# Performance work log

Hardware: AMD Instinct MI355X
Metric: run time of the kernel (lower is better)

Reference implementation:

```python
import jax, jax.numpy as jnp
import numpy as np

B, L, HID = 4, 1024, 768
H, D = 12, 64  # num heads, head dim (HID = H*D)


def setup_inputs() -> dict:
    key = jax.random.key(0)
    ks = jax.random.split(key, 8)
    s = 0.02
    return {
        "hidden_states": jax.random.normal(ks[0], (B, L, HID), jnp.float32),
        "attention_mask": jnp.zeros((B, 1, 1, L), jnp.float32),
        "structure_matrix": jax.random.normal(ks[1], (L, L, D), jnp.float32) * s,
        "Wq": jax.random.normal(ks[2], (HID, HID), jnp.float32) * s,
        "bq": jnp.zeros((HID,), jnp.float32),
        "Wk": jax.random.normal(ks[3], (HID, HID), jnp.float32) * s,
        "bk": jnp.zeros((HID,), jnp.float32),
        "Wv": jax.random.normal(ks[4], (HID, HID), jnp.float32) * s,
        "bv": jnp.zeros((HID,), jnp.float32),
    }


def _heads(x):
    # [B, L, HID] -> [B, H, L, D]
    return x.reshape(B, L, H, D).transpose(0, 2, 1, 3)


def reference(hidden_states, attention_mask, structure_matrix, Wq, bq, Wk, bk, Wv, bv):
    q = _heads(hidden_states @ Wq.T + bq)  # bhld
    k = _heads(hidden_states @ Wk.T + bk)
    v = _heads(hidden_states @ Wv.T + bv)
    scores = jnp.einsum('bhld,bhrd->bhlr', q, k)
    # structure bias: query-side and key-side position-pair terms
    scores = scores + jnp.einsum('bhld,lrd->bhlr', q, structure_matrix)
    scores = scores + jnp.einsum('bhrd,lrd->bhlr', k, structure_matrix)
    scores = scores / jnp.sqrt(jnp.asarray(D, scores.dtype))
    scores = scores + attention_mask
    probs = jax.nn.softmax(scores, axis=-1)
    ctx = jnp.einsum('bhlr,bhrd->bhld', probs, v)
    return ctx.transpose(0, 2, 1, 3).reshape(B, L, HID)
```

## Files before the change

### kernel.cpp

```cpp
#include <hip/hip_runtime.h>

#define BATCH 4
#define SEQ   1024
#define HIDN  768
#define NH    12
#define HD    64
#define BHN   48

typedef __attribute__((ext_vector_type(8))) short bf16x8;
typedef __attribute__((ext_vector_type(4))) float f32x4;

#define MFMA(a, b, c) __builtin_amdgcn_mfma_f32_16x16x32_bf16((a), (b), (c), 0, 0, 0)

__device__ inline unsigned short f2bf(float f) {
    union { float f; unsigned u; } v; v.f = f;
    unsigned r = (v.u + 0x7FFFu + ((v.u >> 16) & 1u)) >> 16;
    return (unsigned short)r;
}
__device__ inline float bf2f(unsigned short s) {
    union { unsigned u; float f; } v; v.u = ((unsigned)s) << 16;
    return v.f;
}
__device__ inline unsigned long long pack4(float a, float b, float c, float d) {
    return (unsigned long long)f2bf(a)
         | ((unsigned long long)f2bf(b) << 16)
         | ((unsigned long long)f2bf(c) << 32)
         | ((unsigned long long)f2bf(d) << 48);
}

__global__ __launch_bounds__(256) void qkv_kernel(
    const float* __restrict__ hidden,
    const float* __restrict__ Wq, const float* __restrict__ bq,
    const float* __restrict__ Wk, const float* __restrict__ bk,
    const float* __restrict__ Wv, const float* __restrict__ bv,
    unsigned short* __restrict__ Qb, unsigned short* __restrict__ Kb,
    unsigned short* __restrict__ Vb)
{
    const int mt  = blockIdx.x;
    const int nt  = blockIdx.y;
    const int mat = blockIdx.z;
    const float* W  = (mat == 0) ? Wq : (mat == 1) ? Wk : Wv;
    const float* bs = (mat == 0) ? bq : (mat == 1) ? bk : bv;
    unsigned short* out = (mat == 0) ? Qb : (mat == 1) ? Kb : Vb;

    const int t = threadIdx.x, lane = t & 63, wid = t >> 6;
    const int row16 = lane & 15, kg = lane >> 4;
    const int m0 = mt * 128;
    const int wm = (wid >> 1) * 64, wn = (wid & 1) * 32;

    __shared__ __align__(16) unsigned short As[128 * 40];
    __shared__ __align__(16) unsigned short Ws[64 * 40];

    f32x4 acc[4][2] = {};

    for (int k0 = 0; k0 < HIDN; k0 += 32) {
        for (int i = 0; i < 4; ++i) {
            int f4 = t + i * 256;
            int r = f4 >> 3, c4 = f4 & 7;
            float4 v = *(const float4*)(hidden + (size_t)(m0 + r) * HIDN + k0 + c4 * 4);
            *(unsigned long long*)&As[r * 40 + c4 * 4] = pack4(v.x, v.y, v.z, v.w);
        }
        for (int i = 0; i < 2; ++i) {
            int f4 = t + i * 256;
            int r = f4 >> 3, c4 = f4 & 7;
            float4 v = *(const float4*)(W + (size_t)(nt * 64 + r) * HIDN + k0 + c4 * 4);
            *(unsigned long long*)&Ws[r * 40 + c4 * 4] = pack4(v.x, v.y, v.z, v.w);
        }
        __syncthreads();
        bf16x8 af[4], bfr[2];
        for (int mf = 0; mf < 4; ++mf)
            af[mf] = *(const bf16x8*)&As[(wm + mf * 16 + row16) * 40 + kg * 8];
        for (int nf = 0; nf < 2; ++nf)
            bfr[nf] = *(const bf16x8*)&Ws[(wn + nf * 16 + row16) * 40 + kg * 8];
        for (int mf = 0; mf < 4; ++mf)
            for (int nf = 0; nf < 2; ++nf)
                acc[mf][nf] = MFMA(af[mf], bfr[nf], acc[mf][nf]);
        __syncthreads();
    }

    const int bh = (m0 / SEQ) * NH + nt;
    for (int nf = 0; nf < 2; ++nf) {
        int d = wn + nf * 16 + row16;
        float bias_v = bs[nt * 64 + d];
        for (int mf = 0; mf < 4; ++mf)
            for (int j = 0; j < 4; ++j) {
                int m = m0 + wm + mf * 16 + kg * 4 + j;
                int l = m & (SEQ - 1);
                out[((size_t)bh * SEQ + l) * HD + d] = f2bf(acc[mf][nf][j] + bias_v);
            }
    }
}

__global__ __launch_bounds__(512) void scores_kernel(
    const float* __restrict__ sm, const float* __restrict__ mask,
    const unsigned short* __restrict__ Qb, const unsigned short* __restrict__ Kb,
    float* __restrict__ S)
{
    const int rt = blockIdx.x, lt = blockIdx.y;
    const int r0 = rt * 32, l0 = lt * 16;
    const int t = threadIdx.x, lane = t & 63, wid = t >> 6;
    const int row16 = lane & 15, kg = lane >> 4;

    __shared__ __align__(16) unsigned short sm_s[16 * 32 * 64];
    __shared__ __align__(16) unsigned short bias_s[16 * 32 * 48];
    __shared__ float mask_s[BATCH * 32];

    for (int i = 0; i < 16; ++i) {
        int f4 = t + i * 512;
        int l = f4 >> 9;
        int rem = f4 & 511;
        int r = rem >> 4, d4 = rem & 15;
        float4 v = *(const float4*)(sm + ((size_t)(l0 + l) * SEQ + (r0 + r)) * HD + d4 * 4);
        int idx = (((l * 32 + r) * 64) + d4 * 4) ^ ((((l ^ r) & 7) << 3));
        *(unsigned long long*)&sm_s[idx] = pack4(v.x, v.y, v.z, v.w);
    }
    if (t < BATCH * 32) {
        int b = t >> 5, r = t & 31;
        mask_s[t] = mask[(size_t)b * SEQ + r0 + r];
    }
    __syncthreads();

    for (int li = 0; li < 2; ++li) {
        int l = wid * 2 + li;
        bf16x8 af[2][2];
        for (int mf = 0; mf < 2; ++mf)
            for (int kf = 0; kf < 2; ++kf) {
                int r = mf * 16 + row16, d0 = kf * 32 + kg * 8;
                af[mf][kf] = *(const bf16x8*)&sm_s[(((l * 32 + r) * 64) + d0) ^ ((((l ^ r) & 7) << 3))];
            }
        bf16x8 bq8[3][2];
        for (int nf = 0; nf < 3; ++nf)
            for (int kf = 0; kf < 2; ++kf) {
                int bh = nf * 16 + row16, d0 = kf * 32 + kg * 8;
                bq8[nf][kf] = *(const bf16x8*)&Qb[((size_t)bh * SEQ + l0 + l) * HD + d0];
            }
        f32x4 acc[2][3] = {};
        for (int kf = 0; kf < 2; ++kf)
            for (int mf = 0; mf < 2; ++mf)
                for (int nf = 0; nf < 3; ++nf)
                    acc[mf][nf] = MFMA(af[mf][kf], bq8[nf][kf], acc[mf][nf]);
        for (int mf = 0; mf < 2; ++mf)
            for (int nf = 0; nf < 3; ++nf)
                for (int j = 0; j < 4; ++j) {
                    int r = mf * 16 + kg * 4 + j, bh = nf * 16 + row16;
                    bias_s[(l * 32 + r) * 48 + bh] = f2bf(acc[mf][nf][j]);
                }
    }
    __syncthreads();

    for (int ri = 0; ri < 4; ++ri) {
        int r = wid * 4 + ri;
        bf16x8 af[2];
        for (int kf = 0; kf < 2; ++kf) {
            int l = row16, d0 = kf * 32 + kg * 8;
            af[kf] = *(const bf16x8*)&sm_s[(((l * 32 + r) * 64) + d0) ^ ((((l ^ r) & 7) << 3))];
        }
        bf16x8 bk8[3][2];
        for (int nf = 0; nf < 3; ++nf)
            for (int kf = 0; kf < 2; ++kf) {
                int bh = nf * 16 + row16, d0 = kf * 32 + kg * 8;
                bk8[nf][kf] = *(const bf16x8*)&Kb[((size_t)bh * SEQ + r0 + r) * HD + d0];
            }
        f32x4 acc[3] = {};
        for (int kf = 0; kf < 2; ++kf)
            for (int nf = 0; nf < 3; ++nf)
                acc[nf] = MFMA(af[kf], bk8[nf][kf], acc[nf]);
        for (int nf = 0; nf < 3; ++nf)
            for (int j = 0; j < 4; ++j) {
                int l = kg * 4 + j, bh = nf * 16 + row16;
                int idx = (l * 32 + r) * 48 + bh;
                bias_s[idx] = f2bf(bf2f(bias_s[idx]) + acc[nf][j]);
            }
    }
    __syncthreads();

    for (int bi = 0; bi < 6; ++bi) {
        int bh = wid * 6 + bi;
        int b = bh / NH;
        bf16x8 aq[2], bkf[2][2];
        for (int kf = 0; kf < 2; ++kf)
            aq[kf] = *(const bf16x8*)&Qb[((size_t)bh * SEQ + l0 + row16) * HD + kf * 32 + kg * 8];
        for (int nf = 0; nf < 2; ++nf)
            for (int kf = 0; kf < 2; ++kf)
                bkf[nf][kf] = *(const bf16x8*)&Kb[((size_t)bh * SEQ + r0 + nf * 16 + row16) * HD + kf * 32 + kg * 8];
        f32x4 acc[2] = {};
        for (int kf = 0; kf < 2; ++kf)
            for (int nf = 0; nf < 2; ++nf)
                acc[nf] = MFMA(aq[kf], bkf[nf][kf], acc[nf]);
        for (int nf = 0; nf < 2; ++nf) {
            int r = nf * 16 + row16;
            for (int j = 0; j < 4; ++j) {
                int l = kg * 4 + j;
                float s = (acc[nf][j] + bf2f(bias_s[(l * 32 + r) * 48 + bh])) * 0.125f
                        + mask_s[b * 32 + r];
                S[((size_t)bh * SEQ + l0 + l) * SEQ + r0 + r] = s;
            }
        }
    }
}

__global__ __launch_bounds__(256) void softmax_kernel(float* __restrict__ S)
{
    const int row = blockIdx.x;
    float* base = S + (size_t)row * SEQ;
    const int t = threadIdx.x;

    float4 v = ((const float4*)base)[t];
    float m = fmaxf(fmaxf(v.x, v.y), fmaxf(v.z, v.w));
    for (int off = 32; off; off >>= 1) m = fmaxf(m, __shfl_xor(m, off));
    __shared__ float red[4], red2[4];
    if ((t & 63) == 0) red[t >> 6] = m;
    __syncthreads();
    m = fmaxf(fmaxf(red[0], red[1]), fmaxf(red[2], red[3]));

    float e0 = __expf(v.x - m), e1 = __expf(v.y - m);
    float e2 = __expf(v.z - m), e3 = __expf(v.w - m);
    float s = e0 + e1 + e2 + e3;
    for (int off = 32; off; off >>= 1) s += __shfl_xor(s, off);
    if ((t & 63) == 0) red2[t >> 6] = s;
    __syncthreads();
    s = red2[0] + red2[1] + red2[2] + red2[3];
    float inv = 1.0f / s;

    ((unsigned long long*)base)[t] = pack4(e0 * inv, e1 * inv, e2 * inv, e3 * inv);
}

__global__ __launch_bounds__(256) void pv_kernel(
    const float* __restrict__ Sbuf, const unsigned short* __restrict__ Vb,
    float* __restrict__ out)
{
    const int bh = blockIdx.x;
    const int l0 = blockIdx.y * 128;
    const int b = bh / NH, h = bh % NH;
    const int t = threadIdx.x, lane = t & 63, wid = t >> 6;
    const int row16 = lane & 15, kg = lane >> 4;
    const int wm = (wid >> 1) * 64, wn = (wid & 1) * 32;

    __shared__ __align__(16) unsigned short pt[128 * 72];
    __shared__ __align__(16) unsigned short vt[64 * 72];
    const unsigned short* P = (const unsigned short*)Sbuf;

    f32x4 acc[4][2] = {};
    for (int r0 = 0; r0 < SEQ; r0 += 64) {
        for (int i = 0; i < 8; ++i) {
            int f4 = t + i * 256;
            int row = f4 >> 4, c4 = f4 & 15;
            *(unsigned long long*)&pt[row * 72 + c4 * 4] =
                *(const unsigned long long*)&P[((size_t)(bh * SEQ + l0 + row)) * 2048 + r0 + c4 * 4];
        }
        for (int i = 0; i < 4; ++i) {
            int f4 = t + i * 256;
            int r = f4 >> 4, c4 = f4 & 15;
            unsigned long long pk =
                *(const unsigned long long*)&Vb[((size_t)bh * SEQ + r0 + r) * HD + c4 * 4];
            vt[(c4 * 4 + 0) * 72 + r] = (unsigned short)(pk);
            vt[(c4 * 4 + 1) * 72 + r] = (unsigned short)(pk >> 16);
            vt[(c4 * 4 + 2) * 72 + r] = (unsigned short)(pk >> 32);
            vt[(c4 * 4 + 3) * 72 + r] = (unsigned short)(pk >> 48);
        }
        __syncthreads();
        for (int kf = 0; kf < 2; ++kf) {
            int kk = kf * 32 + kg * 8;
            bf16x8 af[4], bfr[2];
            for (int mf = 0; mf < 4; ++mf)
                af[mf] = *(const bf16x8*)&pt[(wm + mf * 16 + row16) * 72 + kk];
            for (int nf = 0; nf < 2; ++nf)
                bfr[nf] = *(const bf16x8*)&vt[(wn + nf * 16 + row16) * 72 + kk];
            for (int mf = 0; mf < 4; ++mf)
                for (int nf = 0; nf < 2; ++nf)
                    acc[mf][nf] = MFMA(af[mf], bfr[nf], acc[mf][nf]);
        }
        __syncthreads();
    }

    for (int nf = 0; nf < 2; ++nf) {
        int d = wn + nf * 16 + row16;
        for (int mf = 0; mf < 4; ++mf)
            for (int j = 0; j < 4; ++j) {
                int l = l0 + wm + mf * 16 + kg * 4 + j;
                out[((size_t)(b * SEQ + l)) * HIDN + h * HD + d] = acc[mf][nf][j];
            }
    }
}

extern "C" void kernel_launch(void* const* d_in, const int* in_sizes, int n_in,
                              void* d_out, int out_size, void* d_ws, size_t ws_size,
                              hipStream_t stream)
{
    const float* hidden = (const float*)d_in[0];
    const float* mask   = (const float*)d_in[1];
    const float* smat   = (const float*)d_in[2];
    const float* Wq = (const float*)d_in[3];
    const float* bq = (const float*)d_in[4];
    const float* Wk = (const float*)d_in[5];
    const float* bk = (const float*)d_in[6];
    const float* Wv = (const float*)d_in[7];
    const float* bv = (const float*)d_in[8];
    float* out = (float*)d_out;

    char* ws = (char*)d_ws;
    unsigned short* Qb = (unsigned short*)(ws);
    unsigned short* Kb = (unsigned short*)(ws + 6291456);
    unsigned short* Vb = (unsigned short*)(ws + 12582912);
    float* S = (float*)(ws + 18874368);

    qkv_kernel<<<dim3(32, 12, 3), 256, 0, stream>>>(hidden, Wq, bq, Wk, bk, Wv, bv, Qb, Kb, Vb);
    scores_kernel<<<dim3(32, 64), 512, 0, stream>>>(smat, mask, Qb, Kb, S);
    softmax_kernel<<<dim3(BHN * SEQ), 256, 0, stream>>>(S);
    pv_kernel<<<dim3(BHN, 8), 256, 0, stream>>>(S, Vb, out);
}
```

Before: 688.9 us.

## Fuse softmax into PV kernel and shrink scores tile to 16x16

Softmax is merged into the P·V kernel: each block reads 16 fp32 score rows, normalizes them in registers, and keeps bf16 probabilities in a swizzled LDS tile. This removes the separate softmax pass and its bf16 write and re-read of P. V tiles are double-buffered in LDS. The scores kernel tile drops from 32 to 16 key columns with a transposed, padded bias layout and an occupancy hint, doubling the grid. The cost is that V is re-staged by 64 small blocks per head instead of 8, and each PV block does far less MFMA work.

```diff
diff --git a/kernel.cpp b/kernel.cpp
--- a/kernel.cpp
+++ b/kernel.cpp
@@ -91,69 +91,66 @@
     }
 }
 
-__global__ __launch_bounds__(512) void scores_kernel(
+__global__ __launch_bounds__(512, 4) void scores_kernel(
     const float* __restrict__ sm, const float* __restrict__ mask,
     const unsigned short* __restrict__ Qb, const unsigned short* __restrict__ Kb,
     float* __restrict__ S)
 {
     const int rt = blockIdx.x, lt = blockIdx.y;
-    const int r0 = rt * 32, l0 = lt * 16;
+    const int r0 = rt * 16, l0 = lt * 16;
     const int t = threadIdx.x, lane = t & 63, wid = t >> 6;
     const int row16 = lane & 15, kg = lane >> 4;
 
-    __shared__ __align__(16) unsigned short sm_s[16 * 32 * 64];
-    __shared__ __align__(16) unsigned short bias_s[16 * 32 * 48];
-    __shared__ float mask_s[BATCH * 32];
-
-    for (int i = 0; i < 16; ++i) {
+    __shared__ __align__(16) unsigned short sm_s[16 * 16 * 64];
+    __shared__ __align__(16) unsigned short bias_s[16 * 48 * 18];
+    __shared__ float mask_s[BATCH * 16];
+
+    for (int i = 0; i < 8; ++i) {
         int f4 = t + i * 512;
-        int l = f4 >> 9;
-        int rem = f4 & 511;
+        int l = f4 >> 8;
+        int rem = f4 & 255;
         int r = rem >> 4, d4 = rem & 15;
         float4 v = *(const float4*)(sm + ((size_t)(l0 + l) * SEQ + (r0 + r)) * HD + d4 * 4);
-        int idx = (((l * 32 + r) * 64) + d4 * 4) ^ ((((l ^ r) & 7) << 3));
+        int idx = ((l * 16 + r) * 64 + d4 * 4) ^ (((l ^ r) & 7) << 3);
         *(unsigned long long*)&sm_s[idx] = pack4(v.x, v.y, v.z, v.w);
     }
-    if (t < BATCH * 32) {
-        int b = t >> 5, r = t & 31;
+    if (t < BATCH * 16) {
+        int b = t >> 4, r = t & 15;
         mask_s[t] = mask[(size_t)b * SEQ + r0 + r];
     }
     __syncthreads();
 
     for (int li = 0; li < 2; ++li) {
         int l = wid * 2 + li;
-        bf16x8 af[2][2];
-        for (int mf = 0; mf < 2; ++mf)
-            for (int kf = 0; kf < 2; ++kf) {
-                int r = mf * 16 + row16, d0 = kf * 32 + kg * 8;
-                af[mf][kf] = *(const bf16x8*)&sm_s[(((l * 32 + r) * 64) + d0) ^ ((((l ^ r) & 7) << 3))];
-            }
+        bf16x8 af[2];
+        for (int kf = 0; kf < 2; ++kf) {
+            int d0 = kf * 32 + kg * 8;
+            af[kf] = *(const bf16x8*)&sm_s[((l * 16 + row16) * 64 + d0) ^ (((l ^ row16) & 7) << 3)];
+        }
         bf16x8 bq8[3][2];
         for (int nf = 0; nf < 3; ++nf)
             for (int kf = 0; kf < 2; ++kf) {
                 int bh = nf * 16 + row16, d0 = kf * 32 + kg * 8;
                 bq8[nf][kf] = *(const bf16x8*)&Qb[((size_t)bh * SEQ + l0 + l) * HD + d0];
             }
-        f32x4 acc[2][3] = {};
+        f32x4 acc[3] = {};
         for (int kf = 0; kf < 2; ++kf)
-            for (int mf = 0; mf < 2; ++mf)
-                for (int nf = 0; nf < 3; ++nf)
-                    acc[mf][nf] = MFMA(af[mf][kf], bq8[nf][kf], acc[mf][nf]);
-        for (int mf = 0; mf < 2; ++mf)
             for (int nf = 0; nf < 3; ++nf)
-                for (int j = 0; j < 4; ++j) {
-                    int r = mf * 16 + kg * 4 + j, bh = nf * 16 + row16;
-                    bias_s[(l * 32 + r) * 48 + bh] = f2bf(acc[mf][nf][j]);
-                }
-    }
-    __syncthreads();
-
-    for (int ri = 0; ri < 4; ++ri) {
-        int r = wid * 4 + ri;
+                acc[nf] = MFMA(af[kf], bq8[nf][kf], acc[nf]);
+        for (int nf = 0; nf < 3; ++nf)
+            for (int j = 0; j < 4; ++j) {
+                int r = kg * 4 + j, bh = nf * 16 + row16;
+                bias_s[(l * 48 + bh) * 18 + r] = f2bf(acc[nf][j]);
+            }
+    }
+    __syncthreads();
+
+    for (int ri = 0; ri < 2; ++ri) {
+        int r = wid * 2 + ri;
         bf16x8 af[2];
         for (int kf = 0; kf < 2; ++kf) {
-            int l = row16, d0 = kf * 32 + kg * 8;
-            af[kf] = *(const bf16x8*)&sm_s[(((l * 32 + r) * 64) + d0) ^ ((((l ^ r) & 7) << 3))];
+            int d0 = kf * 32 + kg * 8;
+            af[kf] = *(const bf16x8*)&sm_s[((row16 * 16 + r) * 64 + d0) ^ (((row16 ^ r) & 7) << 3)];
         }
         bf16x8 bk8[3][2];
         for (int nf = 0; nf < 3; ++nf)
@@ -168,7 +165,7 @@
         for (int nf = 0; nf < 3; ++nf)
             for (int j = 0; j < 4; ++j) {
                 int l = kg * 4 + j, bh = nf * 16 + row16;
-                int idx = (l * 32 + r) * 48 + bh;
+                int idx = (l * 48 + bh) * 18 + r;
                 bias_s[idx] = f2bf(bf2f(bias_s[idx]) + acc[nf][j]);
             }
     }
@@ -177,109 +174,95 @@
     for (int bi = 0; bi < 6; ++bi) {
         int bh = wid * 6 + bi;
         int b = bh / NH;
-        bf16x8 aq[2], bkf[2][2];
-        for (int kf = 0; kf < 2; ++kf)
-            aq[kf] = *(const bf16x8*)&Qb[((size_t)bh * SEQ + l0 + row16) * HD + kf * 32 + kg * 8];
-        for (int nf = 0; nf < 2; ++nf)
-            for (int kf = 0; kf < 2; ++kf)
-                bkf[nf][kf] = *(const bf16x8*)&Kb[((size_t)bh * SEQ + r0 + nf * 16 + row16) * HD + kf * 32 + kg * 8];
-        f32x4 acc[2] = {};
-        for (int kf = 0; kf < 2; ++kf)
-            for (int nf = 0; nf < 2; ++nf)
-                acc[nf] = MFMA(aq[kf], bkf[nf][kf], acc[nf]);
-        for (int nf = 0; nf < 2; ++nf) {
-            int r = nf * 16 + row16;
-            for (int j = 0; j < 4; ++j) {
-                int l = kg * 4 + j;
-                float s = (acc[nf][j] + bf2f(bias_s[(l * 32 + r) * 48 + bh])) * 0.125f
-                        + mask_s[b * 32 + r];
-                S[((size_t)bh * SEQ + l0 + l) * SEQ + r0 + r] = s;
-            }
-        }
-    }
-}
-
-__global__ __launch_bounds__(256) void softmax_kernel(float* __restrict__ S)
-{
-    const int row = blockIdx.x;
-    float* base = S + (size_t)row * SEQ;
-    const int t = threadIdx.x;
-
-    float4 v = ((const float4*)base)[t];
-    float m = fmaxf(fmaxf(v.x, v.y), fmaxf(v.z, v.w));
-    for (int off = 32; off; off >>= 1) m = fmaxf(m, __shfl_xor(m, off));
-    __shared__ float red[4], red2[4];
-    if ((t & 63) == 0) red[t >> 6] = m;
-    __syncthreads();
-    m = fmaxf(fmaxf(red[0], red[1]), fmaxf(red[2], red[3]));
-
-    float e0 = __expf(v.x - m), e1 = __expf(v.y - m);
-    float e2 = __expf(v.z - m), e3 = __expf(v.w - m);
-    float s = e0 + e1 + e2 + e3;
-    for (int off = 32; off; off >>= 1) s += __shfl_xor(s, off);
-    if ((t & 63) == 0) red2[t >> 6] = s;
-    __syncthreads();
-    s = red2[0] + red2[1] + red2[2] + red2[3];
-    float inv = 1.0f / s;
-
-    ((unsigned long long*)base)[t] = pack4(e0 * inv, e1 * inv, e2 * inv, e3 * inv);
-}
-
-__global__ __launch_bounds__(256) void pv_kernel(
-    const float* __restrict__ Sbuf, const unsigned short* __restrict__ Vb,
+        bf16x8 aq[2], bkf[2];
+        for (int kf = 0; kf < 2; ++kf) {
+            int d0 = kf * 32 + kg * 8;
+            aq[kf]  = *(const bf16x8*)&Qb[((size_t)bh * SEQ + l0 + row16) * HD + d0];
+            bkf[kf] = *(const bf16x8*)&Kb[((size_t)bh * SEQ + r0 + row16) * HD + d0];
+        }
+        f32x4 acc = {};
+        acc = MFMA(aq[0], bkf[0], acc);
+        acc = MFMA(aq[1], bkf[1], acc);
+        for (int j = 0; j < 4; ++j) {
+            int l = kg * 4 + j, r = row16;
+            float s = (acc[j] + bf2f(bias_s[(l * 48 + bh) * 18 + r])) * 0.125f
+                    + mask_s[b * 16 + r];
+            S[((size_t)bh * SEQ + l0 + l) * SEQ + r0 + r] = s;
+        }
+    }
+}
+
+__global__ __launch_bounds__(256, 3) void softpv_kernel(
+    const float* __restrict__ S, const unsigned short* __restrict__ Vb,
     float* __restrict__ out)
 {
-    const int bh = blockIdx.x;
-    const int l0 = blockIdx.y * 128;
+    const int bh = blockIdx.x, lt = blockIdx.y;
+    const int l0 = lt * 16;
     const int b = bh / NH, h = bh % NH;
     const int t = threadIdx.x, lane = t & 63, wid = t >> 6;
     const int row16 = lane & 15, kg = lane >> 4;
-    const int wm = (wid >> 1) * 64, wn = (wid & 1) * 32;
-
-    __shared__ __align__(16) unsigned short pt[128 * 72];
-    __shared__ __align__(16) unsigned short vt[64 * 72];
-    const unsigned short* P = (const unsigned short*)Sbuf;
-
-    f32x4 acc[4][2] = {};
-    for (int r0 = 0; r0 < SEQ; r0 += 64) {
-        for (int i = 0; i < 8; ++i) {
-            int f4 = t + i * 256;
-            int row = f4 >> 4, c4 = f4 & 15;
-            *(unsigned long long*)&pt[row * 72 + c4 * 4] =
-                *(const unsigned long long*)&P[((size_t)(bh * SEQ + l0 + row)) * 2048 + r0 + c4 * 4];
-        }
-        for (int i = 0; i < 4; ++i) {
-            int f4 = t + i * 256;
-            int r = f4 >> 4, c4 = f4 & 15;
-            unsigned long long pk =
-                *(const unsigned long long*)&Vb[((size_t)bh * SEQ + r0 + r) * HD + c4 * 4];
-            vt[(c4 * 4 + 0) * 72 + r] = (unsigned short)(pk);
-            vt[(c4 * 4 + 1) * 72 + r] = (unsigned short)(pk >> 16);
-            vt[(c4 * 4 + 2) * 72 + r] = (unsigned short)(pk >> 32);
-            vt[(c4 * 4 + 3) * 72 + r] = (unsigned short)(pk >> 48);
+
+    __shared__ __align__(16) unsigned short P_s[16 * 1024];
+    __shared__ __align__(16) unsigned short vt[2][64 * 72];
+
+    for (int li = 0; li < 4; ++li) {
+        int l = wid * 4 + li;
+        const float* row = S + ((size_t)bh * SEQ + l0 + l) * SEQ;
+        float4 v0 = ((const float4*)row)[lane];
+        float4 v1 = ((const float4*)row)[lane + 64];
+        float4 v2 = ((const float4*)row)[lane + 128];
+        float4 v3 = ((const float4*)row)[lane + 192];
+        float m = fmaxf(fmaxf(fmaxf(v0.x, v0.y), fmaxf(v0.z, v0.w)),
+                  fmaxf(fmaxf(fmaxf(v1.x, v1.y), fmaxf(v1.z, v1.w)),
+                  fmaxf(fmaxf(fmaxf(v2.x, v2.y), fmaxf(v2.z, v2.w)),
+                        fmaxf(fmaxf(v3.x, v3.y), fmaxf(v3.z, v3.w)))));
+        for (int off = 32; off; off >>= 1) m = fmaxf(m, __shfl_xor(m, off));
+        v0.x = __expf(v0.x - m); v0.y = __expf(v0.y - m); v0.z = __expf(v0.z - m); v0.w = __expf(v0.w - m);
+        v1.x = __expf(v1.x - m); v1.y = __expf(v1.y - m); v1.z = __expf(v1.z - m); v1.w = __expf(v1.w - m);
+        v2.x = __expf(v2.x - m); v2.y = __expf(v2.y - m); v2.z = __expf(v2.z - m); v2.w = __expf(v2.w - m);
+        v3.x = __expf(v3.x - m); v3.y = __expf(v3.y - m); v3.z = __expf(v3.z - m); v3.w = __expf(v3.w - m);
+        float s = (v0.x + v0.y + v0.z + v0.w) + (v1.x + v1.y + v1.z + v1.w)
+                + (v2.x + v2.y + v2.z + v2.w) + (v3.x + v3.y + v3.z + v3.w);
+        for (int off = 32; off; off >>= 1) s += __shfl_xor(s, off);
+        float inv = 1.0f / s;
+        int swz = (l & 7) << 3, base = l << 10;
+        *(unsigned long long*)&P_s[base + (((lane      ) * 4) ^ swz)] = pack4(v0.x*inv, v0.y*inv, v0.z*inv, v0.w*inv);
+        *(unsigned long long*)&P_s[base + (((lane +  64) * 4) ^ swz)] = pack4(v1.x*inv, v1.y*inv, v1.z*inv, v1.w*inv);
+        *(unsigned long long*)&P_s[base + (((lane + 128) * 4) ^ swz)] = pack4(v2.x*inv, v2.y*inv, v2.z*inv, v2.w*inv);
+        *(unsigned long long*)&P_s[base + (((lane + 192) * 4) ^ swz)] = pack4(v3.x*inv, v3.y*inv, v3.z*inv, v3.w*inv);
+    }
+
+    #define STAGE_V(buf, r0v)                                                          \
+        for (int i = 0; i < 4; ++i) {                                                  \
+            int f4 = t + i * 256;                                                      \
+            int r = f4 >> 4, c4 = f4 & 15;                                             \
+            unsigned long long pk =                                                    \
+                *(const unsigned long long*)&Vb[((size_t)bh * SEQ + (r0v) + r) * HD + c4 * 4]; \
+            vt[buf][(c4 * 4 + 0) * 72 + r] = (unsigned short)(pk);                     \
+            vt[buf][(c4 * 4 + 1) * 72 + r] = (unsigned short)(pk >> 16);               \
+            vt[buf][(c4 * 4 + 2) * 72 + r] = (unsigned short)(pk >> 32);               \
+            vt[buf][(c4 * 4 + 3) * 72 + r] = (unsigned short)(pk >> 48);               \
+        }
+
+    STAGE_V(0, 0)
+    __syncthreads();
+
+    f32x4 acc = {};
+    for (int it = 0; it < 16; ++it) {
+        if (it < 15) { STAGE_V((it + 1) & 1, (it + 1) * 64) }
+        int r0 = it * 64, cur = it & 1;
+        for (int kf = 0; kf < 2; ++kf) {
+            int kk = r0 + kf * 32 + kg * 8;
+            bf16x8 a  = *(const bf16x8*)&P_s[(row16 << 10) + (kk ^ ((row16 & 7) << 3))];
+            bf16x8 bv = *(const bf16x8*)&vt[cur][(wid * 16 + row16) * 72 + kf * 32 + kg * 8];
+            acc = MFMA(a, bv, acc);
         }
         __syncthreads();
-        for (int kf = 0; kf < 2; ++kf) {
-            int kk = kf * 32 + kg * 8;
-            bf16x8 af[4], bfr[2];
-            for (int mf = 0; mf < 4; ++mf)
-                af[mf] = *(const bf16x8*)&pt[(wm + mf * 16 + row16) * 72 + kk];
-            for (int nf = 0; nf < 2; ++nf)
-                bfr[nf] = *(const bf16x8*)&vt[(wn + nf * 16 + row16) * 72 + kk];
-            for (int mf = 0; mf < 4; ++mf)
-                for (int nf = 0; nf < 2; ++nf)
-                    acc[mf][nf] = MFMA(af[mf], bfr[nf], acc[mf][nf]);
-        }
-        __syncthreads();
-    }
-
-    for (int nf = 0; nf < 2; ++nf) {
-        int d = wn + nf * 16 + row16;
-        for (int mf = 0; mf < 4; ++mf)
-            for (int j = 0; j < 4; ++j) {
-                int l = l0 + wm + mf * 16 + kg * 4 + j;
-                out[((size_t)(b * SEQ + l)) * HIDN + h * HD + d] = acc[mf][nf][j];
-            }
+    }
+
+    for (int j = 0; j < 4; ++j) {
+        int l = l0 + kg * 4 + j, d = wid * 16 + row16;
+        out[((size_t)b * SEQ + l) * HIDN + h * HD + d] = acc[j];
     }
 }
 
@@ -305,7 +288,6 @@
     float* S = (float*)(ws + 18874368);
 
     qkv_kernel<<<dim3(32, 12, 3), 256, 0, stream>>>(hidden, Wq, bq, Wk, bk, Wv, bv, Qb, Kb, Vb);
-    scores_kernel<<<dim3(32, 64), 512, 0, stream>>>(smat, mask, Qb, Kb, S);
-    softmax_kernel<<<dim3(BHN * SEQ), 256, 0, stream>>>(S);
-    pv_kernel<<<dim3(BHN, 8), 256, 0, stream>>>(S, Vb, out);
-}
+    scores_kernel<<<dim3(64, 64), 512, 0, stream>>>(smat, mask, Qb, Kb, S);
+    softpv_kernel<<<dim3(BHN, 64), 256, 0, stream>>>(S, Vb, out);
+}
```

Result: slower. 730.9 us (+6.1%).
